# Kernel optimization log

Measured on AMD Instinct MI355X. Metric: run time of the kernel, lower is better.

## Reference

```python
import jax, jax.numpy as jnp
import numpy as np

N, NF, D, GH, E, B = 4096, 128, 64, 64, 32768, 32
NG, STEPS = 3, 3  # n_gcn, set2set processing steps


def setup_inputs() -> dict:
    key = jax.random.key(0)
    ks = iter(jax.random.split(key, 64))
    nrm = lambda shape: jax.random.normal(next(ks), shape, dtype=jnp.float32) * 0.05
    inp = {
        'x': jax.random.normal(next(ks), (N, NF), dtype=jnp.float32),
        'edge_attr': jax.random.uniform(next(ks), (E,), dtype=jnp.float32),
        'edge_idx': jax.random.randint(next(ks), (2, E), 0, N),
        'batch_map': jnp.sort(jax.random.randint(next(ks), (N,), 0, B)),
        # pre-GC MLP: NF->D, D->D, D->D (ReLU each)
        'pre_W0': nrm((NF, D)), 'pre_b0': nrm((D,)),
        'pre_W1': nrm((D, D)), 'pre_b1': nrm((D,)),
        'pre_W2': nrm((D, D)), 'pre_b2': nrm((D,)),
        # NNConv edge nets (stacked over NG layers): 1->GH->D*D
        'enn_W1': nrm((NG, 1, GH)), 'enn_b1': nrm((NG, GH)),
        'enn_W2': nrm((NG, GH, D * D)), 'enn_b2': nrm((NG, D * D)),
        'root_W': nrm((NG, D, D)), 'conv_b': nrm((NG, D)),
        # GRU(D, D) per layer, gate order r,z,n (torch), stored transposed for x@W
        'gru_Wih': nrm((NG, D, 3 * D)), 'gru_Whh': nrm((NG, D, 3 * D)),
        'gru_bih': nrm((NG, 3 * D)), 'gru_bhh': nrm((NG, 3 * D)),
        # Set2Set LSTM: input 2D -> hidden D, gate order i,f,g,o (torch)
        's2s_Wih': nrm((2 * D, 4 * D)), 's2s_Whh': nrm((D, 4 * D)),
        's2s_bih': nrm((4 * D,)), 's2s_bhh': nrm((4 * D,)),
        # post-GC MLP: 2D->D, D->D, D->D (ReLU each), then D->1
        'post_W0': nrm((2 * D, D)), 'post_b0': nrm((D,)),
        'post_W1': nrm((D, D)), 'post_b1': nrm((D,)),
        'post_W2': nrm((D, D)), 'post_b2': nrm((D,)),
        'post_W3': nrm((D, 1)), 'post_b3': nrm((1,)),
    }
    return inp


def _forward(x, edge_attr, pre_W0, pre_b0, pre_W1, pre_b1, pre_W2, pre_b2,
             enn_W1, enn_b1, enn_W2, enn_b2, root_W, conv_b,
             gru_Wih, gru_Whh, gru_bih, gru_bhh,
             s2s_Wih, s2s_Whh, s2s_bih, s2s_bhh,
             post_W0, post_b0, post_W1, post_b1, post_W2, post_b2,
             post_W3, post_b3, edge_idx, batch_map):
    relu, sig = jax.nn.relu, jax.nn.sigmoid
    # pre-GC layers
    out = relu(x @ pre_W0 + pre_b0)
    out = relu(out @ pre_W1 + pre_b1)
    out = relu(out @ pre_W2 + pre_b2)  # [N, D]

    src, dst = edge_idx[0], edge_idx[1]
    deg = jax.ops.segment_sum(jnp.ones((E,), out.dtype), dst, num_segments=N)
    deg = jnp.maximum(deg, 1.0)
    ea = edge_attr[:, None]  # view(-1, 1)

    for l in range(NG):
        h = out
        # NNConv: per-edge weight matrix from edge MLP
        We = relu(ea @ enn_W1[l] + enn_b1[l])              # [E, GH]
        We = (We @ enn_W2[l] + enn_b2[l]).reshape(E, D, D)  # [E, D, D]
        msg = jnp.einsum('ei,eio->eo', out[src], We)        # [E, D]
        agg = jax.ops.segment_sum(msg, dst, num_segments=N) / deg[:, None]
        conv = relu(agg + out @ root_W[l] + conv_b[l])
        # single-step GRU update (torch gate order r, z, n)
        gi = conv @ gru_Wih[l] + gru_bih[l]
        gh = h @ gru_Whh[l] + gru_bhh[l]
        i_r, i_z, i_n = jnp.split(gi, 3, axis=-1)
        h_r, h_z, h_n = jnp.split(gh, 3, axis=-1)
        r = sig(i_r + h_r)
        z = sig(i_z + h_z)
        n = jnp.tanh(i_n + r * h_n)
        out = (1.0 - z) * n + z * h

    # Set2Set pooling (early)
    q_star = jnp.zeros((B, 2 * D), out.dtype)
    hh = jnp.zeros((B, D), out.dtype)
    cc = jnp.zeros((B, D), out.dtype)
    for _ in range(STEPS):
        gates = q_star @ s2s_Wih + s2s_bih + hh @ s2s_Whh + s2s_bhh
        gi_, gf, gg, go = jnp.split(gates, 4, axis=-1)
        cc = sig(gf) * cc + sig(gi_) * jnp.tanh(gg)
        hh = sig(go) * jnp.tanh(cc)
        q = hh
        e = jnp.sum(out * q[batch_map], axis=-1)                    # [N]
        m = jax.ops.segment_max(e, batch_map, num_segments=B)
        a = jnp.exp(e - m[batch_map])
        den = jax.ops.segment_sum(a, batch_map, num_segments=B)
        a = a / den[batch_map]
        r_read = jax.ops.segment_sum(a[:, None] * out, batch_map, num_segments=B)
        q_star = jnp.concatenate([q, r_read], axis=-1)              # [B, 2D]

    # post-GC layers
    y = relu(q_star @ post_W0 + post_b0)
    y = relu(y @ post_W1 + post_b1)
    y = relu(y @ post_W2 + post_b2)
    y = y @ post_W3 + post_b3  # [B, 1]
    return y


def reference(x, edge_attr, edge_idx, batch_map, pre_W0, pre_b0, pre_W1, pre_b1,
              pre_W2, pre_b2, enn_W1, enn_b1, enn_W2, enn_b2, root_W, conv_b,
              gru_Wih, gru_Whh, gru_bih, gru_bhh, s2s_Wih, s2s_Whh, s2s_bih,
              s2s_bhh, post_W0, post_b0, post_W1, post_b1, post_W2, post_b2,
              post_W3, post_b3):
    return _forward(x, edge_attr, pre_W0, pre_b0, pre_W1, pre_b1, pre_W2, pre_b2,
                    enn_W1, enn_b1, enn_W2, enn_b2, root_W, conv_b,
                    gru_Wih, gru_Whh, gru_bih, gru_bhh,
                    s2s_Wih, s2s_Whh, s2s_bih, s2s_bhh,
                    post_W0, post_b0, post_W1, post_b1, post_W2, post_b2,
                    post_W3, post_b3, edge_idx, batch_map)
```

## Files before the change

kernel.cpp:

```cpp
#include <hip/hip_runtime.h>
#include <hip/hip_bf16.h>
#include <string.h>

#define NN   4096
#define NE   32768
#define NB   32
#define BKT  64
#define MSG_CHUNK 8

typedef __attribute__((ext_vector_type(8))) short short8;
typedef __attribute__((ext_vector_type(4))) float f4;

__device__ __forceinline__ float sigf(float x) { return 1.0f / (1.0f + __expf(-x)); }
__device__ __forceinline__ short f2bf(float f) {
    __hip_bfloat16 h = __float2bfloat16(f);
    short s;
    memcpy(&s, &h, sizeof(short));
    return s;
}

__global__ __launch_bounds__(256) void k_prep(const float* __restrict__ x,
        const float* __restrict__ W0, const float* __restrict__ b0,
        const float* __restrict__ W1, const float* __restrict__ b1,
        const float* __restrict__ W2, const float* __restrict__ b2,
        const float* __restrict__ enn_W2, __hip_bfloat16* __restrict__ W2F,
        const int* __restrict__ eidx, const float* __restrict__ ea,
        const float* __restrict__ Wih, const float* __restrict__ Whh,
        float* __restrict__ WihT, float* __restrict__ WhhT,
        float* __restrict__ out, float* __restrict__ agg,
        int* cnt_src, int* cnt_dst, int* csr_dst, float* csr_ea) {
    int bid = blockIdx.x, t = threadIdx.x;
    if (bid < 192) {
        __shared__ __hip_bfloat16 tile[4096];
        size_t base = (size_t)bid * 4096;
        for (int i = t; i < 4096; i += 256) {
            int k = i >> 6, o = i & 63;
            int pos = ((o >> 4) << 10) | ((k >> 5) << 9) | (((k >> 3) & 3) << 7)
                    | ((o & 15) << 3) | (k & 7);
            tile[pos] = __float2bfloat16(enn_W2[base + i]);
        }
        __syncthreads();
        for (int i = t; i < 4096; i += 256) W2F[base + i] = tile[i];
    } else if (bid < 320) {
        int e = (bid - 192) * 256 + t;
        int s = eidx[e];
        int d = eidx[NE + e];
        int slot = atomicAdd(&cnt_src[s], 1);
        if (slot < BKT) {
            csr_dst[s * BKT + slot] = d;
            csr_ea[s * BKT + slot] = ea[e];
        }
        atomicAdd(&cnt_dst[d], 1);
    } else if (bid < 352) {
        int c0 = (bid - 320) * 8;
        for (int i = t; i < 1024; i += 256) {
            int c = c0 + (i >> 7), j = i & 127;
            WihT[(size_t)c * 128 + j] = Wih[(size_t)j * 256 + c];
        }
        for (int i = t; i < 512; i += 256) {
            int c = c0 + (i >> 6), j = i & 63;
            WhhT[(size_t)c * 64 + j] = Whh[(size_t)j * 256 + c];
        }
    } else {
        __shared__ float xr[4][128], ha[4][64], hb[4][64];
        int w = t >> 6, j = t & 63;
        int n = (bid - 352) * 4 + w;
        xr[w][j] = x[(size_t)n * 128 + j];
        xr[w][64 + j] = x[(size_t)n * 128 + 64 + j];
        agg[(size_t)n * 64 + j] = 0.f;
        float s = b0[j];
        #pragma unroll 8
        for (int k = 0; k < 128; ++k) s = fmaf(xr[w][k], W0[k * 64 + j], s);
        ha[w][j] = fmaxf(s, 0.f);
        s = b1[j];
        #pragma unroll 8
        for (int k = 0; k < 64; ++k) s = fmaf(ha[w][k], W1[k * 64 + j], s);
        hb[w][j] = fmaxf(s, 0.f);
        s = b2[j];
        #pragma unroll 8
        for (int k = 0; k < 64; ++k) s = fmaf(hb[w][k], W2[k * 64 + j], s);
        out[(size_t)n * 64 + j] = fmaxf(s, 0.f);
    }
}

__global__ __launch_bounds__(256, 4) void k_fused(const float* __restrict__ out,
        const __hip_bfloat16* __restrict__ W2F_l, const float* __restrict__ b2l,
        const float* __restrict__ W1l, const float* __restrict__ b1l,
        const int* __restrict__ cnt_src, const int* __restrict__ csr_dst,
        const float* __restrict__ csr_ea, float* __restrict__ agg) {
    __shared__ __hip_bfloat16 Pt[8 * 2048];
    __shared__ float outs[8][68];
    __shared__ float wlds[4][MSG_CHUNK][32];
    int t = threadIdx.x, wave = t >> 6, lane = t & 63;
    int laneM = lane & 15, quad = lane >> 4;
    int ntile = blockIdx.x >> 1, gc = blockIdx.x & 1;
    int n0 = ntile * 8;
    for (int i = t; i < 512; i += 256) outs[i >> 6][i & 63] = out[(size_t)n0 * 64 + i];
    __syncthreads();
    short8 a0, a1;
    {
        const float* ar = &outs[laneM & 7][quad * 8];
        #pragma unroll
        for (int j = 0; j < 8; ++j) a0[j] = f2bf(ar[j]);
        const float* ar2 = &outs[laneM & 7][32 + quad * 8];
        #pragma unroll
        for (int j = 0; j < 8; ++j) a1[j] = f2bf(ar2[j]);
    }
    float btr[2] = {0.f, 0.f};
    if (gc == 0) {
        for (int k = 0; k < 64; ++k) {
            float bv = b2l[k * 64 + lane];
            #pragma unroll
            for (int u = 0; u < 2; ++u) btr[u] = fmaf(outs[wave * 2 + u][k], bv, btr[u]);
        }
    }
    #pragma unroll
    for (int gp = 0; gp < 4; ++gp) {
        int glA = wave * 8 + gp * 2;
        int gA = gc * 32 + glA;
        const __hip_bfloat16* BgA = W2F_l + (size_t)gA * 4096;
        const __hip_bfloat16* BgB = BgA + 4096;
        int c = wave;
        int p = gp;
        char* wb = (char*)Pt + (quad << 14) + (c << 10) + (laneM << 4)
                 + (((p ^ quad) & 3) << 2);
        #pragma unroll
        for (int sub = 0; sub < 4; ++sub) {
            short8 bA0 = *(const short8*)(BgA + sub * 1024 + lane * 8);
            short8 bA1 = *(const short8*)(BgA + sub * 1024 + 512 + lane * 8);
            short8 bB0 = *(const short8*)(BgB + sub * 1024 + lane * 8);
            short8 bB1 = *(const short8*)(BgB + sub * 1024 + 512 + lane * 8);
            f4 accA = {0.f, 0.f, 0.f, 0.f}, accB = {0.f, 0.f, 0.f, 0.f};
            accA = __builtin_amdgcn_mfma_f32_16x16x32_bf16(a0, bA0, accA, 0, 0, 0);
            accA = __builtin_amdgcn_mfma_f32_16x16x32_bf16(a1, bA1, accA, 0, 0, 0);
            accB = __builtin_amdgcn_mfma_f32_16x16x32_bf16(a0, bB0, accB, 0, 0, 0);
            accB = __builtin_amdgcn_mfma_f32_16x16x32_bf16(a1, bB1, accB, 0, 0, 0);
            if (quad < 2) {
                char* wbs = wb + (sub << 8);
                #pragma unroll
                for (int r = 0; r < 4; ++r) {
                    unsigned pk = (unsigned)(unsigned short)f2bf(accA[r])
                                | ((unsigned)(unsigned short)f2bf(accB[r]) << 16);
                    *(unsigned*)(wbs + (r << 12)) = pk;
                }
            }
        }
    }
    __syncthreads();
    float w1v = (lane < 32) ? W1l[gc * 32 + lane] : 0.f;
    float b1v = (lane < 32) ? b1l[gc * 32 + lane] : 0.f;
    for (int u = 0; u < 2; ++u) {
        int nloc = wave * 2 + u;
        int n = n0 + nloc;
        int deg = cnt_src[n];
        if (deg > BKT) deg = BKT;
        if (deg <= 0) continue;
        int wq = nloc >> 2;
        float preg[32];
        const char* Pn = (const char*)Pt + (nloc << 12);
        #pragma unroll
        for (int c2 = 0; c2 < 4; ++c2) {
            uint4 vv = *(const uint4*)(Pn + (c2 << 10) + (lane << 4));
            unsigned d0 = vv.x, d1 = vv.y, d2 = vv.z, d3 = vv.w;
            if (wq & 1) { unsigned tt = d0; d0 = d1; d1 = tt; tt = d2; d2 = d3; d3 = tt; }
            union { unsigned u2; float f; } cv;
            cv.u2 = d0 << 16;          preg[c2 * 8 + 0] = cv.f;
            cv.u2 = d0 & 0xFFFF0000u;  preg[c2 * 8 + 1] = cv.f;
            cv.u2 = d1 << 16;          preg[c2 * 8 + 2] = cv.f;
            cv.u2 = d1 & 0xFFFF0000u;  preg[c2 * 8 + 3] = cv.f;
            cv.u2 = d2 << 16;          preg[c2 * 8 + 4] = cv.f;
            cv.u2 = d2 & 0xFFFF0000u;  preg[c2 * 8 + 5] = cv.f;
            cv.u2 = d3 << 16;          preg[c2 * 8 + 6] = cv.f;
            cv.u2 = d3 & 0xFFFF0000u;  preg[c2 * 8 + 7] = cv.f;
        }
        float bt = btr[u];
        const int* bdst = csr_dst + n * BKT;
        const float* bea = csr_ea + n * BKT;
        for (int c0 = 0; c0 < deg; c0 += MSG_CHUNK) {
            int cc = deg - c0;
            if (cc > MSG_CHUNK) cc = MSG_CHUNK;
            int dl = 0; float el = 0.f;
            if (lane < cc) { dl = bdst[c0 + lane]; el = bea[c0 + lane]; }
            for (int si = 0; si < cc; ++si) {
                float eav = __shfl(el, si, 64);
                if (lane < 32)
                    wlds[wave][si][lane] = fmaxf(fmaf(eav, w1v, b1v), 0.f);
            }
            for (int i = 0; i < cc; ++i) {
                int dst = __shfl(dl, i, 64);
                const float* wr = wlds[wave][i];
                float acc0 = bt, acc1 = 0.f, acc2 = 0.f, acc3 = 0.f;
                #pragma unroll
                for (int g = 0; g < 32; g += 16) {
                    float4 w0 = *(const float4*)(wr + g);
                    float4 w1 = *(const float4*)(wr + g + 4);
                    float4 w2 = *(const float4*)(wr + g + 8);
                    float4 w3 = *(const float4*)(wr + g + 12);
                    acc0 = fmaf(w0.x, preg[g], acc0);
                    acc0 = fmaf(w0.y, preg[g + 1], acc0);
                    acc0 = fmaf(w0.z, preg[g + 2], acc0);
                    acc0 = fmaf(w0.w, preg[g + 3], acc0);
                    acc1 = fmaf(w1.x, preg[g + 4], acc1);
                    acc1 = fmaf(w1.y, preg[g + 5], acc1);
                    acc1 = fmaf(w1.z, preg[g + 6], acc1);
                    acc1 = fmaf(w1.w, preg[g + 7], acc1);
                    acc2 = fmaf(w2.x, preg[g + 8], acc2);
                    acc2 = fmaf(w2.y, preg[g + 9], acc2);
                    acc2 = fmaf(w2.z, preg[g + 10], acc2);
                    acc2 = fmaf(w2.w, preg[g + 11], acc2);
                    acc3 = fmaf(w3.x, preg[g + 12], acc3);
                    acc3 = fmaf(w3.y, preg[g + 13], acc3);
                    acc3 = fmaf(w3.z, preg[g + 14], acc3);
                    acc3 = fmaf(w3.w, preg[g + 15], acc3);
                }
                float acc = (acc0 + acc1) + (acc2 + acc3);
                atomicAdd(&agg[(size_t)dst * 64 + lane], acc);
            }
        }
    }
}

__global__ __launch_bounds__(256) void k_gru(const float* __restrict__ out,
        float* __restrict__ agg, const int* __restrict__ cnt_dst,
        const float* __restrict__ rootW, const float* __restrict__ convb,
        const float* __restrict__ Wih, const float* __restrict__ Whh,
        const float* __restrict__ bih, const float* __restrict__ bhh,
        float* __restrict__ outn) {
    __shared__ float sh[4][64], sc[4][64];
    int t = threadIdx.x, w = t >> 6, j = t & 63;
    int n = blockIdx.x * 4 + w;
    float hj = out[(size_t)n * 64 + j];
    sh[w][j] = hj;
    int dg = cnt_dst[n];
    float invd = 1.0f / (float)(dg > 0 ? dg : 1);
    float av = agg[(size_t)n * 64 + j];
    agg[(size_t)n * 64 + j] = 0.f;
    __syncthreads();
    float s = av * invd + convb[j];
    #pragma unroll 8
    for (int k = 0; k < 64; ++k) s = fmaf(sh[w][k], rootW[k * 64 + j], s);
    float conv = fmaxf(s, 0.f);
    sc[w][j] = conv;
    __syncthreads();
    float gir = bih[j], giz = bih[64 + j], gin = bih[128 + j];
    float ghr = bhh[j], ghz = bhh[64 + j], ghn = bhh[128 + j];
    #pragma unroll 4
    for (int k = 0; k < 64; ++k) {
        float c = sc[w][k], h = sh[w][k];
        gir = fmaf(c, Wih[k * 192 + j], gir);
        giz = fmaf(c, Wih[k * 192 + 64 + j], giz);
        gin = fmaf(c, Wih[k * 192 + 128 + j], gin);
        ghr = fmaf(h, Whh[k * 192 + j], ghr);
        ghz = fmaf(h, Whh[k * 192 + 64 + j], ghz);
        ghn = fmaf(h, Whh[k * 192 + 128 + j], ghn);
    }
    float r = sigf(gir + ghr);
    float z = sigf(giz + ghz);
    float nn = tanhf(gin + r * ghn);
    outn[(size_t)n * 64 + j] = (1.f - z) * nn + z * hj;
}

__global__ __launch_bounds__(256, 1) void k_s2s_post(const float* __restrict__ out,
        const int* __restrict__ bm,
        const float* __restrict__ WihT, const float* __restrict__ WhhT,
        const float* __restrict__ bih, const float* __restrict__ bhh,
        const float* __restrict__ pW0, const float* __restrict__ pb0,
        const float* __restrict__ pW1, const float* __restrict__ pb1,
        const float* __restrict__ pW2, const float* __restrict__ pb2,
        const float* __restrict__ pW3, const float* __restrict__ pb3,
        float* __restrict__ y) {
    __shared__ float cacheT[64 * 193];
    __shared__ float wpost[16448];
    __shared__ float qs[128];
    __shared__ float hh_l[64];
    __shared__ float gates_l[256];
    __shared__ float ebuf[1024];
    __shared__ float redw[4], redw2[4];
    __shared__ float redbuf[4][64];
    __shared__ float tmp64[64];
    int t = threadIdx.x, wave = t >> 6, lane = t & 63;
    int b = blockIdx.x;
    int s0, e0;
    {
        int lo = 0, hi = NN;
        while (lo < hi) { int mid = (lo + hi) >> 1; if (bm[mid] < b) lo = mid + 1; else hi = mid; }
        s0 = lo;
        hi = NN;
        while (lo < hi) { int mid = (lo + hi) >> 1; if (bm[mid] < b + 1) lo = mid + 1; else hi = mid; }
        e0 = lo;
    }
    int cnt = e0 - s0;
    if (cnt < 0) cnt = 0;
    if (cnt > 1024) cnt = 1024;
    int ccnt = cnt < 192 ? cnt : 192;
    int nf4 = ccnt * 16;
    const float4* out4 = (const float4*)(out + (size_t)s0 * 64);
    float4 stg[12];
    #pragma unroll
    for (int i = 0; i < 12; ++i) {
        int v = t + i * 256;
        if (v < nf4) stg[i] = out4[v];
    }
    #pragma unroll
    for (int i = 0; i < 12; ++i) {
        int v = t + i * 256;
        if (v < nf4) {
            int row = v >> 4, dq = v & 15;
            cacheT[(dq * 4 + 0) * 193 + row] = stg[i].x;
            cacheT[(dq * 4 + 1) * 193 + row] = stg[i].y;
            cacheT[(dq * 4 + 2) * 193 + row] = stg[i].z;
            cacheT[(dq * 4 + 3) * 193 + row] = stg[i].w;
        }
    }
    {
        float4* wp4 = (float4*)wpost;
        #pragma unroll
        for (int i = 0; i < 8; ++i) { int v = t + i * 256; wp4[v] = ((const float4*)pW0)[v]; }
        #pragma unroll
        for (int i = 0; i < 4; ++i) { int v = t + i * 256; wp4[2048 + v] = ((const float4*)pW1)[v]; }
        #pragma unroll
        for (int i = 0; i < 4; ++i) { int v = t + i * 256; wp4[3072 + v] = ((const float4*)pW2)[v]; }
        if (t < 16) wp4[4096 + t] = ((const float4*)pW3)[t];
    }
    const float4* wihT4 = (const float4*)(WihT + (size_t)t * 128);
    const float4* whhT4 = (const float4*)(WhhT + (size_t)t * 64);
    float bsum = bih[t] + bhh[t];
    float ccr = 0.f;
    if (t < 128) qs[t] = 0.f;
    if (t < 64) hh_l[t] = 0.f;
    __syncthreads();
    const float4* qs4 = (const float4*)qs;
    const float4* hh4 = (const float4*)hh_l;
    for (int step = 0; step < 3; ++step) {
        float g0 = bsum, g1 = 0.f, g2 = 0.f, g3 = 0.f;
        #pragma unroll
        for (int jq = 0; jq < 32; ++jq) {
            float4 w = wihT4[jq];
            float4 v = qs4[jq];
            g0 = fmaf(v.x, w.x, g0);
            g1 = fmaf(v.y, w.y, g1);
            g2 = fmaf(v.z, w.z, g2);
            g3 = fmaf(v.w, w.w, g3);
        }
        #pragma unroll
        for (int jq = 0; jq < 16; ++jq) {
            float4 w = whhT4[jq];
            float4 v = hh4[jq];
            g0 = fmaf(v.x, w.x, g0);
            g1 = fmaf(v.y, w.y, g1);
            g2 = fmaf(v.z, w.z, g2);
            g3 = fmaf(v.w, w.w, g3);
        }
        gates_l[t] = (g0 + g1) + (g2 + g3);
        __syncthreads();
        if (t < 64) {
            float cn = sigf(gates_l[64 + t]) * ccr
                     + sigf(gates_l[t]) * tanhf(gates_l[128 + t]);
            ccr = cn;
            hh_l[t] = sigf(gates_l[192 + t]) * tanhf(cn);
        }
        __syncthreads();
        for (int idx = t; idx < cnt; idx += 256) {
            float s0a = 0.f, s1a = 0.f, s2a = 0.f, s3a = 0.f;
            if (idx < 192) {
                #pragma unroll
                for (int dq = 0; dq < 16; ++dq) {
                    float4 h = hh4[dq];
                    s0a = fmaf(cacheT[(dq * 4 + 0) * 193 + idx], h.x, s0a);
                    s1a = fmaf(cacheT[(dq * 4 + 1) * 193 + idx], h.y, s1a);
                    s2a = fmaf(cacheT[(dq * 4 + 2) * 193 + idx], h.z, s2a);
                    s3a = fmaf(cacheT[(dq * 4 + 3) * 193 + idx], h.w, s3a);
                }
            } else {
                const float* row = out + (size_t)(s0 + idx) * 64;
                #pragma unroll
                for (int dq = 0; dq < 16; ++dq) {
                    float4 h = hh4[dq];
                    s0a = fmaf(row[dq * 4 + 0], h.x, s0a);
                    s1a = fmaf(row[dq * 4 + 1], h.y, s1a);
                    s2a = fmaf(row[dq * 4 + 2], h.z, s2a);
                    s3a = fmaf(row[dq * 4 + 3], h.w, s3a);
                }
            }
            ebuf[idx] = (s0a + s1a) + (s2a + s3a);
        }
        __syncthreads();
        float lm = -3.0e38f;
        for (int idx = t; idx < cnt; idx += 256) lm = fmaxf(lm, ebuf[idx]);
        #pragma unroll
        for (int off = 32; off > 0; off >>= 1) lm = fmaxf(lm, __shfl_xor(lm, off, 64));
        if (lane == 0) redw[wave] = lm;
        __syncthreads();
        float m = fmaxf(fmaxf(redw[0], redw[1]), fmaxf(redw[2], redw[3]));
        float ls = 0.f;
        for (int idx = t; idx < cnt; idx += 256) {
            float a = __expf(ebuf[idx] - m);
            ebuf[idx] = a;
            ls += a;
        }
        #pragma unroll
        for (int off = 32; off > 0; off >>= 1) ls += __shfl_xor(ls, off, 64);
        if (lane == 0) redw2[wave] = ls;
        __syncthreads();
        float ssum = (redw2[0] + redw2[1]) + (redw2[2] + redw2[3]);
        float inv = (cnt > 0) ? 1.f / ssum : 0.f;
        float r0 = 0.f;
        for (int row = wave; row < ccnt; row += 4)
            r0 = fmaf(ebuf[row], cacheT[lane * 193 + row], r0);
        for (int row = 192 + wave; row < cnt; row += 4)
            r0 = fmaf(ebuf[row], out[(size_t)(s0 + row) * 64 + lane], r0);
        redbuf[wave][lane] = r0;
        __syncthreads();
        if (t < 64) {
            float s = ((redbuf[0][t] + redbuf[1][t]) + (redbuf[2][t] + redbuf[3][t]));
            qs[64 + t] = s * inv;
            qs[t] = hh_l[t];
        }
        __syncthreads();
    }
    if (t < 64) {
        float s = pb0[t];
        #pragma unroll 4
        for (int k = 0; k < 128; ++k) s = fmaf(qs[k], wpost[k * 64 + t], s);
        tmp64[t] = fmaxf(s, 0.f);
    }
    __syncthreads();
    float h1v = 0.f;
    if (t < 64) {
        float s = pb1[t];
        #pragma unroll 4
        for (int k = 0; k < 64; ++k) s = fmaf(tmp64[k], wpost[8192 + k * 64 + t], s);
        h1v = fmaxf(s, 0.f);
    }
    __syncthreads();
    if (t < 64) tmp64[t] = h1v;
    __syncthreads();
    if (t < 64) {
        float s = pb2[t];
        #pragma unroll 4
        for (int k = 0; k < 64; ++k) s = fmaf(tmp64[k], wpost[12288 + k * 64 + t], s);
        gates_l[t] = fmaxf(s, 0.f) * wpost[16384 + t];
    }
    __syncthreads();
    if (t == 0) {
        float yy = pb3[0];
        for (int k = 0; k < 64; ++k) yy += gates_l[k];
        y[b] = yy;
    }
}


extern "C" void kernel_launch(void* const* d_in, const int* in_sizes, int n_in,
                              void* d_out, int out_size, void* d_ws, size_t ws_size,
                              hipStream_t stream) {
    const float* x         = (const float*)d_in[0];
    const float* edge_attr = (const float*)d_in[1];
    const int*   edge_idx  = (const int*)d_in[2];
    const int*   batch_map = (const int*)d_in[3];
    const float* pre_W0 = (const float*)d_in[4];
    const float* pre_b0 = (const float*)d_in[5];
    const float* pre_W1 = (const float*)d_in[6];
    const float* pre_b1 = (const float*)d_in[7];
    const float* pre_W2 = (const float*)d_in[8];
    const float* pre_b2 = (const float*)d_in[9];
    const float* enn_W1 = (const float*)d_in[10];
    const float* enn_b1 = (const float*)d_in[11];
    const float* enn_W2 = (const float*)d_in[12];
    const float* enn_b2 = (const float*)d_in[13];
    const float* root_W = (const float*)d_in[14];
    const float* conv_b = (const float*)d_in[15];
    const float* gru_Wih = (const float*)d_in[16];
    const float* gru_Whh = (const float*)d_in[17];
    const float* gru_bih = (const float*)d_in[18];
    const float* gru_bhh = (const float*)d_in[19];
    const float* s2s_Wih = (const float*)d_in[20];
    const float* s2s_Whh = (const float*)d_in[21];
    const float* s2s_bih = (const float*)d_in[22];
    const float* s2s_bhh = (const float*)d_in[23];
    const float* post_W0 = (const float*)d_in[24];
    const float* post_b0 = (const float*)d_in[25];
    const float* post_W1 = (const float*)d_in[26];
    const float* post_b1 = (const float*)d_in[27];
    const float* post_W2 = (const float*)d_in[28];
    const float* post_b2 = (const float*)d_in[29];
    const float* post_W3 = (const float*)d_in[30];
    const float* post_b3 = (const float*)d_in[31];
    float* yout = (float*)d_out;

    char* wp = (char*)d_ws;
    auto take = [&](size_t bytes) -> char* {
        char* r = wp;
        wp += (bytes + 255) & ~(size_t)255;
        return r;
    };
    float* outA = (float*)take((size_t)NN * 64 * 4);
    float* outB = (float*)take((size_t)NN * 64 * 4);
    float* agg  = (float*)take((size_t)NN * 64 * 4);
    __hip_bfloat16* W2F = (__hip_bfloat16*)take((size_t)3 * 64 * 4096 * 2);
    int* cnt_src  = (int*)take((size_t)NN * 4);
    int* cnt_dst  = (int*)take((size_t)NN * 4);
    int* csr_dst  = (int*)take((size_t)NN * BKT * 4);
    float* csr_ea = (float*)take((size_t)NN * BKT * 4);
    float* WihT   = (float*)take((size_t)256 * 128 * 4);
    float* WhhT   = (float*)take((size_t)256 * 64 * 4);

    hipMemsetAsync(cnt_src, 0, (size_t)2 * NN * 4, stream);

    k_prep<<<1376, 256, 0, stream>>>(x, pre_W0, pre_b0, pre_W1, pre_b1, pre_W2, pre_b2,
                                     enn_W2, W2F, edge_idx, edge_attr,
                                     s2s_Wih, s2s_Whh, WihT, WhhT,
                                     outA, agg, cnt_src, cnt_dst, csr_dst, csr_ea);

    float* cur = outA;
    float* nxt = outB;
    for (int l = 0; l < 3; ++l) {
        k_fused<<<NN / 8 * 2, 256, 0, stream>>>(cur, W2F + (size_t)l * 64 * 4096,
                                                enn_b2 + (size_t)l * 4096,
                                                enn_W1 + l * 64, enn_b1 + l * 64,
                                                cnt_src, csr_dst, csr_ea, agg);
        k_gru<<<NN / 4, 256, 0, stream>>>(cur, agg, cnt_dst, root_W + l * 4096,
                                          conv_b + l * 64, gru_Wih + l * 64 * 192,
                                          gru_Whh + l * 64 * 192, gru_bih + l * 192,
                                          gru_bhh + l * 192, nxt);
        float* tmp = cur; cur = nxt; nxt = tmp;
    }
    k_s2s_post<<<NB, 256, 0, stream>>>(cur, batch_map, WihT, WhhT, s2s_bih,
                                       s2s_bhh, post_W0, post_b0, post_W1, post_b1,
                                       post_W2, post_b2, post_W3, post_b3, yout);
}
```

Measured before the change: 311.6 us.

## Fuse GRU update of layer l with message passing of layer l+1

```diff
diff --git a/kernel.cpp b/kernel.cpp
--- a/kernel.cpp
+++ b/kernel.cpp
@@ -27,7 +27,7 @@
         const int* __restrict__ eidx, const float* __restrict__ ea,
         const float* __restrict__ Wih, const float* __restrict__ Whh,
         float* __restrict__ WihT, float* __restrict__ WhhT,
-        float* __restrict__ out, float* __restrict__ agg,
+        float* __restrict__ out, float* __restrict__ aggAll,
         int* cnt_src, int* cnt_dst, int* csr_dst, float* csr_ea) {
     int bid = blockIdx.x, t = threadIdx.x;
     if (bid < 192) {
@@ -67,7 +67,9 @@
         int n = (bid - 352) * 4 + w;
         xr[w][j] = x[(size_t)n * 128 + j];
         xr[w][64 + j] = x[(size_t)n * 128 + 64 + j];
-        agg[(size_t)n * 64 + j] = 0.f;
+        aggAll[(size_t)n * 64 + j] = 0.f;
+        aggAll[(size_t)NN * 64 + (size_t)n * 64 + j] = 0.f;
+        aggAll[(size_t)2 * NN * 64 + (size_t)n * 64 + j] = 0.f;
         float s = b0[j];
         #pragma unroll 8
         for (int k = 0; k < 128; ++k) s = fmaf(xr[w][k], W0[k * 64 + j], s);
@@ -220,6 +222,190 @@
     }
 }
 
+__global__ __launch_bounds__(256, 4) void k_fgru(
+        const float* __restrict__ out_prev, float* __restrict__ out_cur,
+        const float* __restrict__ agg_in, const int* __restrict__ cnt_dst,
+        const float* __restrict__ rootW, const float* __restrict__ convb,
+        const float* __restrict__ gWih, const float* __restrict__ gWhh,
+        const float* __restrict__ gbih, const float* __restrict__ gbhh,
+        const __hip_bfloat16* __restrict__ W2F_l, const float* __restrict__ b2l,
+        const float* __restrict__ W1l, const float* __restrict__ b1l,
+        const int* __restrict__ cnt_src, const int* __restrict__ csr_dst,
+        const float* __restrict__ csr_ea, float* __restrict__ agg_out) {
+    __shared__ __hip_bfloat16 Pt[8 * 2048];
+    __shared__ float outs[8][68];
+    __shared__ float wlds[4][MSG_CHUNK][32];
+    int t = threadIdx.x, wave = t >> 6, lane = t & 63;
+    int laneM = lane & 15, quad = lane >> 4;
+    int ntile = blockIdx.x >> 1, gc = blockIdx.x & 1;
+    int n0 = ntile * 8;
+    int j = lane;
+    for (int i = t; i < 512; i += 256)
+        outs[i >> 6][i & 63] = out_prev[(size_t)n0 * 64 + i];
+    __syncthreads();
+    float* scL = &wlds[0][0][0];
+    for (int u = 0; u < 2; ++u) {
+        int nl = wave * 2 + u;
+        int n = n0 + nl;
+        int dg = cnt_dst[n];
+        float invd = 1.0f / (float)(dg > 0 ? dg : 1);
+        float av = agg_in[(size_t)n * 64 + j];
+        float s = av * invd + convb[j];
+        #pragma unroll 8
+        for (int k = 0; k < 64; ++k) s = fmaf(outs[nl][k], rootW[k * 64 + j], s);
+        scL[nl * 64 + j] = fmaxf(s, 0.f);
+    }
+    __syncthreads();
+    float o_new[2];
+    for (int u = 0; u < 2; ++u) {
+        int nl = wave * 2 + u;
+        float hj = outs[nl][j];
+        float gir = gbih[j], giz = gbih[64 + j], gin = gbih[128 + j];
+        float ghr = gbhh[j], ghz = gbhh[64 + j], ghn = gbhh[128 + j];
+        #pragma unroll 4
+        for (int k = 0; k < 64; ++k) {
+            float c = scL[nl * 64 + k], h = outs[nl][k];
+            gir = fmaf(c, gWih[k * 192 + j], gir);
+            giz = fmaf(c, gWih[k * 192 + 64 + j], giz);
+            gin = fmaf(c, gWih[k * 192 + 128 + j], gin);
+            ghr = fmaf(h, gWhh[k * 192 + j], ghr);
+            ghz = fmaf(h, gWhh[k * 192 + 64 + j], ghz);
+            ghn = fmaf(h, gWhh[k * 192 + 128 + j], ghn);
+        }
+        float r = sigf(gir + ghr);
+        float z = sigf(giz + ghz);
+        float nn2 = tanhf(gin + r * ghn);
+        o_new[u] = (1.f - z) * nn2 + z * hj;
+    }
+    __syncthreads();
+    for (int u = 0; u < 2; ++u) outs[wave * 2 + u][j] = o_new[u];
+    __syncthreads();
+    if (gc == 0)
+        for (int i = t; i < 512; i += 256)
+            out_cur[(size_t)n0 * 64 + i] = outs[i >> 6][i & 63];
+    short8 a0, a1;
+    {
+        const float* ar = &outs[laneM & 7][quad * 8];
+        #pragma unroll
+        for (int q = 0; q < 8; ++q) a0[q] = f2bf(ar[q]);
+        const float* ar2 = &outs[laneM & 7][32 + quad * 8];
+        #pragma unroll
+        for (int q = 0; q < 8; ++q) a1[q] = f2bf(ar2[q]);
+    }
+    float btr[2] = {0.f, 0.f};
+    if (gc == 0) {
+        for (int k = 0; k < 64; ++k) {
+            float bv = b2l[k * 64 + lane];
+            #pragma unroll
+            for (int u = 0; u < 2; ++u) btr[u] = fmaf(outs[wave * 2 + u][k], bv, btr[u]);
+        }
+    }
+    #pragma unroll
+    for (int gp = 0; gp < 4; ++gp) {
+        int glA = wave * 8 + gp * 2;
+        int gA = gc * 32 + glA;
+        const __hip_bfloat16* BgA = W2F_l + (size_t)gA * 4096;
+        const __hip_bfloat16* BgB = BgA + 4096;
+        int c = wave;
+        int p = gp;
+        char* wb = (char*)Pt + (quad << 14) + (c << 10) + (laneM << 4)
+                 + (((p ^ quad) & 3) << 2);
+        #pragma unroll
+        for (int sub = 0; sub < 4; ++sub) {
+            short8 bA0 = *(const short8*)(BgA + sub * 1024 + lane * 8);
+            short8 bA1 = *(const short8*)(BgA + sub * 1024 + 512 + lane * 8);
+            short8 bB0 = *(const short8*)(BgB + sub * 1024 + lane * 8);
+            short8 bB1 = *(const short8*)(BgB + sub * 1024 + 512 + lane * 8);
+            f4 accA = {0.f, 0.f, 0.f, 0.f}, accB = {0.f, 0.f, 0.f, 0.f};
+            accA = __builtin_amdgcn_mfma_f32_16x16x32_bf16(a0, bA0, accA, 0, 0, 0);
+            accA = __builtin_amdgcn_mfma_f32_16x16x32_bf16(a1, bA1, accA, 0, 0, 0);
+            accB = __builtin_amdgcn_mfma_f32_16x16x32_bf16(a0, bB0, accB, 0, 0, 0);
+            accB = __builtin_amdgcn_mfma_f32_16x16x32_bf16(a1, bB1, accB, 0, 0, 0);
+            if (quad < 2) {
+                char* wbs = wb + (sub << 8);
+                #pragma unroll
+                for (int r = 0; r < 4; ++r) {
+                    unsigned pk = (unsigned)(unsigned short)f2bf(accA[r])
+                                | ((unsigned)(unsigned short)f2bf(accB[r]) << 16);
+                    *(unsigned*)(wbs + (r << 12)) = pk;
+                }
+            }
+        }
+    }
+    __syncthreads();
+    float w1v = (lane < 32) ? W1l[gc * 32 + lane] : 0.f;
+    float b1v = (lane < 32) ? b1l[gc * 32 + lane] : 0.f;
+    for (int u = 0; u < 2; ++u) {
+        int nloc = wave * 2 + u;
+        int n = n0 + nloc;
+        int deg = cnt_src[n];
+        if (deg > BKT) deg = BKT;
+        if (deg <= 0) continue;
+        int wq = nloc >> 2;
+        float preg[32];
+        const char* Pn = (const char*)Pt + (nloc << 12);
+        #pragma unroll
+        for (int c2 = 0; c2 < 4; ++c2) {
+            uint4 vv = *(const uint4*)(Pn + (c2 << 10) + (lane << 4));
+            unsigned d0 = vv.x, d1 = vv.y, d2 = vv.z, d3 = vv.w;
+            if (wq & 1) { unsigned tt = d0; d0 = d1; d1 = tt; tt = d2; d2 = d3; d3 = tt; }
+            union { unsigned u2; float f; } cv;
+            cv.u2 = d0 << 16;          preg[c2 * 8 + 0] = cv.f;
+            cv.u2 = d0 & 0xFFFF0000u;  preg[c2 * 8 + 1] = cv.f;
+            cv.u2 = d1 << 16;          preg[c2 * 8 + 2] = cv.f;
+            cv.u2 = d1 & 0xFFFF0000u;  preg[c2 * 8 + 3] = cv.f;
+            cv.u2 = d2 << 16;          preg[c2 * 8 + 4] = cv.f;
+            cv.u2 = d2 & 0xFFFF0000u;  preg[c2 * 8 + 5] = cv.f;
+            cv.u2 = d3 << 16;          preg[c2 * 8 + 6] = cv.f;
+            cv.u2 = d3 & 0xFFFF0000u;  preg[c2 * 8 + 7] = cv.f;
+        }
+        float bt = btr[u];
+        const int* bdst = csr_dst + n * BKT;
+        const float* bea = csr_ea + n * BKT;
+        for (int c0 = 0; c0 < deg; c0 += MSG_CHUNK) {
+            int cc = deg - c0;
+            if (cc > MSG_CHUNK) cc = MSG_CHUNK;
+            int dl = 0; float el = 0.f;
+            if (lane < cc) { dl = bdst[c0 + lane]; el = bea[c0 + lane]; }
+            for (int si = 0; si < cc; ++si) {
+                float eav = __shfl(el, si, 64);
+                if (lane < 32)
+                    wlds[wave][si][lane] = fmaxf(fmaf(eav, w1v, b1v), 0.f);
+            }
+            for (int i = 0; i < cc; ++i) {
+                int dst = __shfl(dl, i, 64);
+                const float* wr = wlds[wave][i];
+                float acc0 = bt, acc1 = 0.f, acc2 = 0.f, acc3 = 0.f;
+                #pragma unroll
+                for (int g = 0; g < 32; g += 16) {
+                    float4 w0 = *(const float4*)(wr + g);
+                    float4 w1 = *(const float4*)(wr + g + 4);
+                    float4 w2 = *(const float4*)(wr + g + 8);
+                    float4 w3 = *(const float4*)(wr + g + 12);
+                    acc0 = fmaf(w0.x, preg[g], acc0);
+                    acc0 = fmaf(w0.y, preg[g + 1], acc0);
+                    acc0 = fmaf(w0.z, preg[g + 2], acc0);
+                    acc0 = fmaf(w0.w, preg[g + 3], acc0);
+                    acc1 = fmaf(w1.x, preg[g + 4], acc1);
+                    acc1 = fmaf(w1.y, preg[g + 5], acc1);
+                    acc1 = fmaf(w1.z, preg[g + 6], acc1);
+                    acc1 = fmaf(w1.w, preg[g + 7], acc1);
+                    acc2 = fmaf(w2.x, preg[g + 8], acc2);
+                    acc2 = fmaf(w2.y, preg[g + 9], acc2);
+                    acc2 = fmaf(w2.z, preg[g + 10], acc2);
+                    acc2 = fmaf(w2.w, preg[g + 11], acc2);
+                    acc3 = fmaf(w3.x, preg[g + 12], acc3);
+                    acc3 = fmaf(w3.y, preg[g + 13], acc3);
+                    acc3 = fmaf(w3.z, preg[g + 14], acc3);
+                    acc3 = fmaf(w3.w, preg[g + 15], acc3);
+                }
+                float acc = (acc0 + acc1) + (acc2 + acc3);
+                atomicAdd(&agg_out[(size_t)dst * 64 + lane], acc);
+            }
+        }
+    }
+}
+
 __global__ __launch_bounds__(256) void k_gru(const float* __restrict__ out,
         float* __restrict__ agg, const int* __restrict__ cnt_dst,
         const float* __restrict__ rootW, const float* __restrict__ convb,
@@ -234,7 +420,6 @@
     int dg = cnt_dst[n];
     float invd = 1.0f / (float)(dg > 0 ? dg : 1);
     float av = agg[(size_t)n * 64 + j];
-    agg[(size_t)n * 64 + j] = 0.f;
     __syncthreads();
     float s = av * invd + convb[j];
     #pragma unroll 8
@@ -495,7 +680,7 @@
     };
     float* outA = (float*)take((size_t)NN * 64 * 4);
     float* outB = (float*)take((size_t)NN * 64 * 4);
-    float* agg  = (float*)take((size_t)NN * 64 * 4);
+    float* aggP = (float*)take((size_t)3 * NN * 64 * 4);
     __hip_bfloat16* W2F = (__hip_bfloat16*)take((size_t)3 * 64 * 4096 * 2);
     int* cnt_src  = (int*)take((size_t)NN * 4);
     int* cnt_dst  = (int*)take((size_t)NN * 4);
@@ -503,28 +688,34 @@
     float* csr_ea = (float*)take((size_t)NN * BKT * 4);
     float* WihT   = (float*)take((size_t)256 * 128 * 4);
     float* WhhT   = (float*)take((size_t)256 * 64 * 4);
+    float* agg0 = aggP;
+    float* agg1 = aggP + (size_t)NN * 64;
+    float* agg2 = aggP + (size_t)2 * NN * 64;
 
     hipMemsetAsync(cnt_src, 0, (size_t)2 * NN * 4, stream);
 
     k_prep<<<1376, 256, 0, stream>>>(x, pre_W0, pre_b0, pre_W1, pre_b1, pre_W2, pre_b2,
                                      enn_W2, W2F, edge_idx, edge_attr,
                                      s2s_Wih, s2s_Whh, WihT, WhhT,
-                                     outA, agg, cnt_src, cnt_dst, csr_dst, csr_ea);
-
-    float* cur = outA;
-    float* nxt = outB;
-    for (int l = 0; l < 3; ++l) {
-        k_fused<<<NN / 8 * 2, 256, 0, stream>>>(cur, W2F + (size_t)l * 64 * 4096,
-                                                enn_b2 + (size_t)l * 4096,
-                                                enn_W1 + l * 64, enn_b1 + l * 64,
-                                                cnt_src, csr_dst, csr_ea, agg);
-        k_gru<<<NN / 4, 256, 0, stream>>>(cur, agg, cnt_dst, root_W + l * 4096,
-                                          conv_b + l * 64, gru_Wih + l * 64 * 192,
-                                          gru_Whh + l * 64 * 192, gru_bih + l * 192,
-                                          gru_bhh + l * 192, nxt);
-        float* tmp = cur; cur = nxt; nxt = tmp;
-    }
-    k_s2s_post<<<NB, 256, 0, stream>>>(cur, batch_map, WihT, WhhT, s2s_bih,
+                                     outA, aggP, cnt_src, cnt_dst, csr_dst, csr_ea);
+
+    k_fused<<<NN / 8 * 2, 256, 0, stream>>>(outA, W2F,
+                                            enn_b2, enn_W1, enn_b1,
+                                            cnt_src, csr_dst, csr_ea, agg0);
+    k_fgru<<<NN / 8 * 2, 256, 0, stream>>>(outA, outB, agg0, cnt_dst,
+        root_W, conv_b, gru_Wih, gru_Whh, gru_bih, gru_bhh,
+        W2F + (size_t)1 * 64 * 4096, enn_b2 + 4096, enn_W1 + 64, enn_b1 + 64,
+        cnt_src, csr_dst, csr_ea, agg1);
+    k_fgru<<<NN / 8 * 2, 256, 0, stream>>>(outB, outA, agg1, cnt_dst,
+        root_W + 4096, conv_b + 64, gru_Wih + 64 * 192, gru_Whh + 64 * 192,
+        gru_bih + 192, gru_bhh + 192,
+        W2F + (size_t)2 * 64 * 4096, enn_b2 + 2 * 4096, enn_W1 + 128, enn_b1 + 128,
+        cnt_src, csr_dst, csr_ea, agg2);
+    k_gru<<<NN / 4, 256, 0, stream>>>(outA, agg2, cnt_dst, root_W + 2 * 4096,
+                                      conv_b + 2 * 64, gru_Wih + 2 * 64 * 192,
+                                      gru_Whh + 2 * 64 * 192, gru_bih + 2 * 192,
+                                      gru_bhh + 2 * 192, outB);
+    k_s2s_post<<<NB, 256, 0, stream>>>(outB, batch_map, WihT, WhhT, s2s_bih,
                                        s2s_bhh, post_W0, post_b0, post_W1, post_b1,
                                        post_W2, post_b2, post_W3, post_b3, yout);
 }
```

Result: slower. 332.9 us (+6.8%).
